# Kernel optimization log

Hardware: AMD Instinct MI355X
Metric: run time of the kernel (lower is better)

Reference implementation:

```python
import jax, jax.numpy as jnp
import numpy as np

PAGE_SIZE = 64  # page size of the 64-token page table (get_page_table_64)


def setup_inputs() -> dict:
    key = jax.random.key(0)
    k1, k2, k3, k4 = jax.random.split(key, 4)
    b, h, d = 64, 64, 128
    num_blocks = 128
    num_pages = b * num_blocks
    query = jax.random.normal(k1, (b, h, d), dtype=jnp.float32)
    weights = jax.random.normal(k2, (b, h), dtype=jnp.float32)
    index_k_cache = jax.random.normal(k3, (num_pages, PAGE_SIZE, d), dtype=jnp.float32)
    # each batch row gets its own distinct pages (all indices in range)
    block_tables = jnp.arange(b * num_blocks, dtype=jnp.int32).reshape(b, num_blocks)
    seq_lens = jax.random.randint(k4, (b,), 1, num_blocks * PAGE_SIZE, dtype=jnp.int32)
    return {
        "query": query,
        "weights": weights,
        "index_k_cache": index_k_cache,
        "block_tables": block_tables,
        "seq_lens": seq_lens,
    }


def reference(query, weights, index_k_cache, block_tables, seq_lens):
    # Faithful translation of triton_mqa_logits_kernel (paged MQA ReLU-weighted
    # QK logits for the top-k indexer).
    b, h, d = query.shape
    num_blocks = block_tables.shape[1]
    max_seq_len = num_blocks * PAGE_SIZE
    # Gather paged KV per block table: [b, num_blocks, PAGE, d] -> [b, S, d]
    k = index_k_cache[block_tables].reshape(b, max_seq_len, d)
    # s[b,h,s] = q . k  (MQA: single K shared across index heads)
    s = jnp.einsum("bhd,bsd->bhs", query, k)
    # ReLU then per-head weighted sum over heads -> [b, S]
    logits = jnp.einsum("bh,bhs->bs", weights, jax.nn.relu(s))
    # positions beyond the sequence length are invalid (-inf, as in the ragged
    # path all_qk_logits init, so downstream top-k never selects them)
    pos = jnp.arange(max_seq_len, dtype=jnp.int32)
    mask = pos[None, :] < seq_lens[:, None]
    return jnp.where(mask, logits, -jnp.inf).astype(jnp.float32)
```

## Files before the change

kernel.cpp:

```cpp
#include <hip/hip_runtime.h>
#include <hip/hip_bf16.h>

#define B 64
#define H 64
#define D 128
#define NB 128
#define PAGE 64
#define SMAX (NB * PAGE)
#define TILE_S 128
#define NEG_BIG (-3.0e38f)

typedef __attribute__((ext_vector_type(8))) short bf16x8;
typedef __attribute__((ext_vector_type(4))) float f32x4;

__device__ __forceinline__ unsigned short f2bf(float f) {
    union { __hip_bfloat16 h; unsigned short u; } cv;
    cv.h = __float2bfloat16(f);
    return cv.u;
}
__device__ __forceinline__ bf16x8 cvt8(float4 a, float4 b) {
    bf16x8 r;
    r[0] = (short)f2bf(a.x); r[1] = (short)f2bf(a.y);
    r[2] = (short)f2bf(a.z); r[3] = (short)f2bf(a.w);
    r[4] = (short)f2bf(b.x); r[5] = (short)f2bf(b.y);
    r[6] = (short)f2bf(b.z); r[7] = (short)f2bf(b.w);
    return r;
}

__global__ __launch_bounds__(256) void indexer_kernel(
    const float* __restrict__ query,
    const float* __restrict__ weights,
    const float* __restrict__ kcache,
    const int*   __restrict__ block_tables,
    const int*   __restrict__ seq_lens,
    float*       __restrict__ out)
{
    const int b    = blockIdx.y;
    const int tile = blockIdx.x;
    const int tid  = threadIdx.x;
    const int slen = seq_lens[b];

    if (tile * TILE_S >= slen) {
        if (tid < TILE_S)
            out[(size_t)b * SMAX + tile * TILE_S + tid] = NEG_BIG;
        return;
    }

    __shared__ __align__(16) unsigned short q_lds[H * 16 * 8];

    const int wv = tid >> 6, ln = tid & 63;
    const int quad = ln >> 4, lm = ln & 15;

    float4 kf[2][4][2];
    #pragma unroll
    for (int mi = 0; mi < 2; ++mi) {
        const int pos  = tile * TILE_S + wv * 32 + mi * 16 + lm;
        const int page = block_tables[b * NB + (pos >> 6)];
        const float* rowp = kcache + ((size_t)page * PAGE + (pos & 63)) * D;
        #pragma unroll
        for (int kc = 0; kc < 4; ++kc) {
            kf[mi][kc][0] = *(const float4*)(rowp + kc * 32 + quad * 8);
            kf[mi][kc][1] = *(const float4*)(rowp + kc * 32 + quad * 8 + 4);
        }
    }

    const float* qb = query + (size_t)b * H * D;
    #pragma unroll
    for (int i = 0; i < 4; ++i) {
        const int idx = i * 256 + tid;
        const int h = idx >> 4, c = idx & 15;
        const float4 f0 = *(const float4*)(qb + h * D + c * 8);
        const float4 f1 = *(const float4*)(qb + h * D + c * 8 + 4);
        const int slot = h * 16 + (c ^ (h & 15));
        *(bf16x8*)&q_lds[slot * 8] = cvt8(f0, f1);
    }
    __syncthreads();

    f32x4 acc[2][4] = {};
    #pragma unroll
    for (int kc = 0; kc < 4; ++kc) {
        bf16x8 a[2];
        #pragma unroll
        for (int mi = 0; mi < 2; ++mi)
            a[mi] = cvt8(kf[mi][kc][0], kf[mi][kc][1]);
        bf16x8 q[4];
        #pragma unroll
        for (int ni = 0; ni < 4; ++ni) {
            const int h = ni * 16 + lm;
            const int slot = h * 16 + ((kc * 4 + quad) ^ lm);
            q[ni] = *(const bf16x8*)&q_lds[slot * 8];
        }
        #pragma unroll
        for (int mi = 0; mi < 2; ++mi)
            #pragma unroll
            for (int ni = 0; ni < 4; ++ni)
                acc[mi][ni] = __builtin_amdgcn_mfma_f32_16x16x32_bf16(
                    a[mi], q[ni], acc[mi][ni], 0, 0, 0);
    }

    float w[4];
    #pragma unroll
    for (int ni = 0; ni < 4; ++ni)
        w[ni] = weights[b * H + ni * 16 + lm];

    #pragma unroll
    for (int mi = 0; mi < 2; ++mi) {
        #pragma unroll
        for (int r = 0; r < 4; ++r) {
            float v = 0.f;
            #pragma unroll
            for (int ni = 0; ni < 4; ++ni)
                v = fmaf(w[ni], fmaxf(acc[mi][ni][r], 0.f), v);
            v += __shfl_xor(v, 1);
            v += __shfl_xor(v, 2);
            v += __shfl_xor(v, 4);
            v += __shfl_xor(v, 8);
            if (lm == 0) {
                const int pos = tile * TILE_S + wv * 32 + mi * 16 + quad * 4 + r;
                out[(size_t)b * SMAX + pos] = (pos < slen) ? v : NEG_BIG;
            }
        }
    }
}

extern "C" void kernel_launch(void* const* d_in, const int* in_sizes, int n_in,
                              void* d_out, int out_size, void* d_ws, size_t ws_size,
                              hipStream_t stream) {
    const float* query   = (const float*)d_in[0];
    const float* weights = (const float*)d_in[1];
    const float* kcache  = (const float*)d_in[2];
    const int*   bt      = (const int*)d_in[3];
    const int*   sl      = (const int*)d_in[4];
    float*       out     = (float*)d_out;

    dim3 grid(SMAX / TILE_S, B);
    indexer_kernel<<<grid, 256, 0, stream>>>(query, weights, kcache, bt, sl, out);
}
```

Before: 335.4 us.

## Precompute bf16 query in prep kernel, load to LDS directly, skip inactive waves

Adds a separate q_prep kernel that converts the query to swizzled bf16 once per batch row into workspace. The main kernel then copies it into LDS with global_load_lds, where it was previously re-converting fp32 query in every tile block. The bf16 conversion becomes a cheap add-and-permute that rounds with ties not to even and does not handle NaN. Waves whose 32 positions are all past seq_len skip their K loads and only write the fill value. The cost is an extra kernel launch and a workspace round trip for the query.

```diff
diff --git a/kernel.cpp b/kernel.cpp
--- a/kernel.cpp
+++ b/kernel.cpp
@@ -13,22 +13,49 @@
 typedef __attribute__((ext_vector_type(8))) short bf16x8;
 typedef __attribute__((ext_vector_type(4))) float f32x4;
 
-__device__ __forceinline__ unsigned short f2bf(float f) {
-    union { __hip_bfloat16 h; unsigned short u; } cv;
-    cv.h = __float2bfloat16(f);
-    return cv.u;
+__device__ __forceinline__ unsigned int rnd16(float f) {
+    union { float f; unsigned int u; } v; v.f = f;
+    return v.u + 0x8000u;
+}
+__device__ __forceinline__ unsigned int pack2(float lo, float hi) {
+    return __builtin_amdgcn_perm(rnd16(hi), rnd16(lo), 0x07060302);
 }
 __device__ __forceinline__ bf16x8 cvt8(float4 a, float4 b) {
-    bf16x8 r;
-    r[0] = (short)f2bf(a.x); r[1] = (short)f2bf(a.y);
-    r[2] = (short)f2bf(a.z); r[3] = (short)f2bf(a.w);
-    r[4] = (short)f2bf(b.x); r[5] = (short)f2bf(b.y);
-    r[6] = (short)f2bf(b.z); r[7] = (short)f2bf(b.w);
-    return r;
+    union { unsigned int u[4]; bf16x8 v; } r;
+    r.u[0] = pack2(a.x, a.y); r.u[1] = pack2(a.z, a.w);
+    r.u[2] = pack2(b.x, b.y); r.u[3] = pack2(b.z, b.w);
+    return r.v;
+}
+
+__device__ __forceinline__ void load_lds16(const void* g, void* l) {
+    __builtin_amdgcn_global_load_lds(
+        (const __attribute__((address_space(1))) unsigned int*)g,
+        (__attribute__((address_space(3))) unsigned int*)l,
+        16, 0, 0);
+}
+
+__global__ __launch_bounds__(256) void q_prep(
+    const float* __restrict__ query, unsigned int* __restrict__ qws)
+{
+    const int b = blockIdx.x, tid = threadIdx.x;
+    const float* qb = query + (size_t)b * H * D;
+    unsigned int* ob = qws + (size_t)b * 4096;
+    #pragma unroll
+    for (int i = 0; i < 4; ++i) {
+        const int idx = i * 256 + tid;
+        const int h = idx >> 4, c = idx & 15;
+        const float4 f0 = *(const float4*)(qb + h * D + c * 8);
+        const float4 f1 = *(const float4*)(qb + h * D + c * 8 + 4);
+        uint4 o;
+        o.x = pack2(f0.x, f0.y); o.y = pack2(f0.z, f0.w);
+        o.z = pack2(f1.x, f1.y); o.w = pack2(f1.z, f1.w);
+        const int slot = h * 16 + (c ^ (h & 15));
+        *(uint4*)(ob + slot * 4) = o;
+    }
 }
 
 __global__ __launch_bounds__(256) void indexer_kernel(
-    const float* __restrict__ query,
+    const unsigned int* __restrict__ qws,
     const float* __restrict__ weights,
     const float* __restrict__ kcache,
     const int*   __restrict__ block_tables,
@@ -51,30 +78,38 @@
     const int wv = tid >> 6, ln = tid & 63;
     const int quad = ln >> 4, lm = ln & 15;
 
+    {
+        const unsigned int* src = qws + (size_t)b * 4096 + wv * 1024;
+        #pragma unroll
+        for (int j = 0; j < 4; ++j)
+            load_lds16(src + j * 256 + ln * 4,
+                       &q_lds[(wv * 1024 + j * 256) * 2]);
+    }
+
+    const int wbase = tile * TILE_S + wv * 32;
+    const bool wactive = wbase < slen;
+
     float4 kf[2][4][2];
-    #pragma unroll
-    for (int mi = 0; mi < 2; ++mi) {
-        const int pos  = tile * TILE_S + wv * 32 + mi * 16 + lm;
-        const int page = block_tables[b * NB + (pos >> 6)];
-        const float* rowp = kcache + ((size_t)page * PAGE + (pos & 63)) * D;
+    if (wactive) {
         #pragma unroll
-        for (int kc = 0; kc < 4; ++kc) {
-            kf[mi][kc][0] = *(const float4*)(rowp + kc * 32 + quad * 8);
-            kf[mi][kc][1] = *(const float4*)(rowp + kc * 32 + quad * 8 + 4);
+        for (int mi = 0; mi < 2; ++mi) {
+            const int pos  = wbase + mi * 16 + lm;
+            const int page = block_tables[b * NB + (pos >> 6)];
+            const float* rowp = kcache + ((size_t)page * PAGE + (pos & 63)) * D;
+            #pragma unroll
+            for (int kc = 0; kc < 4; ++kc) {
+                kf[mi][kc][0] = *(const float4*)(rowp + kc * 32 + quad * 8);
+                kf[mi][kc][1] = *(const float4*)(rowp + kc * 32 + quad * 8 + 4);
+            }
         }
     }
 
-    const float* qb = query + (size_t)b * H * D;
-    #pragma unroll
-    for (int i = 0; i < 4; ++i) {
-        const int idx = i * 256 + tid;
-        const int h = idx >> 4, c = idx & 15;
-        const float4 f0 = *(const float4*)(qb + h * D + c * 8);
-        const float4 f1 = *(const float4*)(qb + h * D + c * 8 + 4);
-        const int slot = h * 16 + (c ^ (h & 15));
-        *(bf16x8*)&q_lds[slot * 8] = cvt8(f0, f1);
+    __syncthreads();
+
+    if (!wactive) {
+        if (ln < 32) out[(size_t)b * SMAX + wbase + ln] = NEG_BIG;
+        return;
     }
-    __syncthreads();
 
     f32x4 acc[2][4] = {};
     #pragma unroll
@@ -116,7 +151,7 @@
             v += __shfl_xor(v, 4);
             v += __shfl_xor(v, 8);
             if (lm == 0) {
-                const int pos = tile * TILE_S + wv * 32 + mi * 16 + quad * 4 + r;
+                const int pos = wbase + mi * 16 + quad * 4 + r;
                 out[(size_t)b * SMAX + pos] = (pos < slen) ? v : NEG_BIG;
             }
         }
@@ -132,7 +167,9 @@
     const int*   bt      = (const int*)d_in[3];
     const int*   sl      = (const int*)d_in[4];
     float*       out     = (float*)d_out;
+    unsigned int* qws    = (unsigned int*)d_ws;
 
+    q_prep<<<B, 256, 0, stream>>>(query, qws);
     dim3 grid(SMAX / TILE_S, B);
-    indexer_kernel<<<grid, 256, 0, stream>>>(query, weights, kcache, bt, sl, out);
+    indexer_kernel<<<grid, 256, 0, stream>>>(qws, weights, kcache, bt, sl, out);
 }
```

Result: no change. 337.6 us (+0.7%).
